# Optimization experiments

Hardware: AMD Instinct MI355X
Metric: run time of the kernel (lower is better)

## Reference

```python
import jax, jax.numpy as jnp
import numpy as np

B, S, D, H, K = 16, 4096, 256, 512, 3
EPS = 1e-5


def setup_inputs() -> dict:
    key = jax.random.key(0)
    ks = jax.random.split(key, 16)
    glorot = lambda k, shape: jax.random.uniform(
        k, shape, jnp.float32, -1.0, 1.0) * np.sqrt(6.0 / (shape[0] + shape[-1]))
    return {
        "inputs": jax.random.normal(ks[0], (B, S, D), jnp.float32),
        "mask": jax.random.randint(ks[1], (B, S), 0, 2, jnp.int32),
        "in_w": glorot(ks[2], (H, D)),
        "in_b": jnp.zeros((H,), jnp.float32),
        "gate_w": glorot(ks[3], (H, D)),
        "gate_b": jnp.zeros((H,), jnp.float32),
        "dw_w": glorot(ks[4], (H, 1, K)),
        "dw_b": jnp.zeros((H,), jnp.float32),
        "pw_w": glorot(ks[5], (H, H, 1)),
        "pw_b": jnp.zeros((H,), jnp.float32),
        "ln_g": jnp.ones((H,), jnp.float32),
        "ln_b": jnp.zeros((H,), jnp.float32),
        "A_log": jax.random.normal(ks[6], (H,), jnp.float32) * -0.1,
        "Bp": jax.random.normal(ks[7], (H,), jnp.float32) * 0.1,
        "Cp": jax.random.normal(ks[8], (H,), jnp.float32) * 0.1,
    }


def _forward(inputs, mask, in_w, in_b, gate_w, gate_b, dw_w, dw_b,
             pw_w, pw_b, ln_g, ln_b, A_log, Bp, Cp):
    # projections: torch Linear is x @ W.T + b
    x_lin = jnp.einsum('bsd,hd->bsh', inputs, in_w) + in_b
    g_lin = jnp.einsum('bsd,hd->bsh', inputs, gate_w) + gate_b
    h = jnp.tanh(x_lin)
    m_f = mask.astype(h.dtype)                      # [B,S]
    h = h * m_f[:, :, None]
    # depthwise conv over time: [B,H,S] with groups=H, 'same' padding
    pad = (K - 1) // 2
    h_t = jnp.transpose(h, (0, 2, 1))               # [B,H,S]
    h_conv = jax.lax.conv_general_dilated(
        h_t, dw_w, window_strides=(1,), padding=[(pad, pad)],
        dimension_numbers=('NCH', 'OIH', 'NCH'), feature_group_count=H)
    h_conv = h_conv + dw_b[None, :, None]
    h_conv = jnp.transpose(h_conv, (0, 2, 1))       # [B,S,H]
    # pointwise 1x1 conv
    h_conv = jnp.einsum('bsh,oh->bso', h_conv, pw_w[:, :, 0]) + pw_b
    u = jax.nn.silu(h_conv + h)
    g = jax.nn.sigmoid(g_lin)
    a_exp = jnp.exp(-jax.nn.softplus(A_log))        # [H]

    def step(carry, xs):
        state, last = carry
        ut, gt, mt = xs                             # [B,H],[B,H],[B]
        new_state = gt * (a_exp * state) + (1.0 - gt) * (Bp * ut)
        keep = (mt > 0.5)[:, None]
        state = jnp.where(keep, new_state, state)
        y = state * Cp
        last = jnp.where(keep, y, last)
        return (state, last), last

    init = (jnp.zeros((B, H), u.dtype), jnp.zeros((B, H), u.dtype))
    xs = (jnp.transpose(u, (1, 0, 2)), jnp.transpose(g, (1, 0, 2)),
          jnp.transpose(m_f, (1, 0)))
    _, y_seq = jax.lax.scan(step, init, xs)         # [S,B,H]
    y_seq = jnp.transpose(y_seq, (1, 0, 2))         # [B,S,H]
    # LayerNorm over last dim
    mu = jnp.mean(y_seq, axis=-1, keepdims=True)
    var = jnp.var(y_seq, axis=-1, keepdims=True)
    return (y_seq - mu) * jax.lax.rsqrt(var + EPS) * ln_g + ln_b


def reference(inputs, mask, in_w, in_b, gate_w, gate_b, dw_w, dw_b,
              pw_w, pw_b, ln_g, ln_b, A_log, Bp, Cp):
    return _forward(inputs, mask, in_w, in_b, gate_w, gate_b, dw_w, dw_b,
                    pw_w, pw_b, ln_g, ln_b, A_log, Bp, Cp)
```

## Files before the change

### kernel.cpp

```cpp
#include <hip/hip_runtime.h>
#include <hip/hip_bf16.h>
#include <math.h>

#define B_  16
#define S_  4096
#define D_  256
#define H_  512
#define BS_ 65536
#define BSH_ 33554432L
#define BSD_ 16777216L
#define CCH 128
#define LCH 32
#define TPAD 136

typedef __bf16 bf16;
typedef __bf16 bf16x8 __attribute__((ext_vector_type(8)));
typedef float  f32x4  __attribute__((ext_vector_type(4)));

#define AS1 __attribute__((address_space(1)))
#define AS3 __attribute__((address_space(3)))

__device__ __forceinline__ void gload_lds16(const void* g, void* l) {
  __builtin_amdgcn_global_load_lds((const AS1 void*)g, (AS3 void*)l, 16, 0, 0);
}

#if __has_builtin(__builtin_amdgcn_exp2f)
#define EXP2F __builtin_amdgcn_exp2f
#else
#define EXP2F exp2f
#endif
#if __has_builtin(__builtin_amdgcn_rcpf)
#define RCPF __builtin_amdgcn_rcpf
#else
#define RCPF(x) (1.f/(x))
#endif
#define L2E 1.4426950408889634f

__device__ __forceinline__ float fsigmoid(float x) {
  return RCPF(1.f + EXP2F(-L2E * x));
}
__device__ __forceinline__ float ftanh(float x) {
  return 2.f * RCPF(1.f + EXP2F(-2.f * L2E * x)) - 1.f;
}
__device__ __forceinline__ float fsilu(float x) {
  return x * RCPF(1.f + EXP2F(-L2E * x));
}

__global__ void k_cast_x(const float* __restrict__ x, bf16* __restrict__ xb, int n8) {
  int i = blockIdx.x * blockDim.x + threadIdx.x;
  if (i >= n8) return;
  const float4* p = (const float4*)x + (long)i * 2;
  float4 a = p[0], b = p[1];
  bf16x8 o;
  o[0]=(bf16)a.x; o[1]=(bf16)a.y; o[2]=(bf16)a.z; o[3]=(bf16)a.w;
  o[4]=(bf16)b.x; o[5]=(bf16)b.y; o[6]=(bf16)b.z; o[7]=(bf16)b.w;
  ((bf16x8*)xb)[i] = o;
}

__global__ void k_cast_w(const float* __restrict__ in_w, const float* __restrict__ gate_w,
                         const float* __restrict__ pw_w,
                         bf16* __restrict__ w1, bf16* __restrict__ pw) {
  int i = blockIdx.x * blockDim.x + threadIdx.x;
  const int HD = H_ * D_;
  if (i < HD)            w1[i] = (bf16)in_w[i];
  else if (i < 2 * HD)   w1[i] = (bf16)gate_w[i - HD];
  else {
    int j = i - 2 * HD;
    if (j < H_ * H_)     pw[j] = (bf16)pw_w[j];
  }
}

template<int KDIM, int EPI>
__global__ __launch_bounds__(512, 5)
void k_gemm(const bf16* __restrict__ A, const bf16* __restrict__ Bw,
            const int* __restrict__ mask,
            const float* __restrict__ bias0, const float* __restrict__ bias1,
            const bf16* __restrict__ hbuf, const bf16* __restrict__ gbuf,
            const float* __restrict__ A_log, const float* __restrict__ Bp,
            float* __restrict__ Ac, float* __restrict__ Bc,
            bf16* __restrict__ out0, bf16* __restrict__ out1, int Ntiles)
{
  extern __shared__ char smem_raw[];
  bf16* tile = (bf16*)smem_raw;

  const int t = threadIdx.x;
  const int w = t >> 6, lane = t & 63;
  const int nwg = gridDim.x;
  const int wg = (blockIdx.x & 7) * (nwg >> 3) + (blockIdx.x >> 3);
  const int bn0 = (wg % Ntiles) * 128;
  const int bm0 = (wg / Ntiles) * 128;
  const int wm = w >> 2, wn = w & 3;
  const int fr = lane & 15, kq = lane >> 4;
  constexpr int NT = KDIM / 32;

  const bf16* Ag = A  + (long)(bm0 + (t >> 2)) * KDIM + (t & 3) * 8;
  const bf16* Bg = Bw + (long)(bn0 + (t >> 2)) * KDIM + (t & 3) * 8;

  f32x4 acc[4][2];
#pragma unroll
  for (int i = 0; i < 4; ++i)
#pragma unroll
    for (int j = 0; j < 2; ++j) acc[i][j] = (f32x4){0.f, 0.f, 0.f, 0.f};

#define STAGE(tt)                                                           \
  { char* _b = smem_raw + ((tt) & 1) * 16384;                               \
    gload_lds16(Ag + (tt) * 32, (bf16*)_b + t * 8);                         \
    gload_lds16(Bg + (tt) * 32, (bf16*)(_b + 8192) + t * 8); }

  STAGE(0); STAGE(1);

#pragma unroll
  for (int kt = 0; kt < NT; ++kt) {
    if (kt + 1 < NT) asm volatile("s_waitcnt vmcnt(2)" ::: "memory");
    else             asm volatile("s_waitcnt vmcnt(0)" ::: "memory");
    __builtin_amdgcn_s_barrier();

    const bf16* As = (const bf16*)(smem_raw + (kt & 1) * 16384);
    const bf16* Bs = As + 4096;
    bf16x8 af[4], bfr[2];
#pragma unroll
    for (int mi = 0; mi < 4; ++mi)
      af[mi] = *(const bf16x8*)&As[(wm * 64 + mi * 16 + fr) * 32 + kq * 8];
#pragma unroll
    for (int ni = 0; ni < 2; ++ni)
      bfr[ni] = *(const bf16x8*)&Bs[(wn * 32 + ni * 16 + fr) * 32 + kq * 8];

    asm volatile("s_waitcnt lgkmcnt(0)" ::: "memory");
    __builtin_amdgcn_s_barrier();

    if (kt + 2 < NT) STAGE(kt + 2);

#pragma unroll
    for (int mi = 0; mi < 4; ++mi)
#pragma unroll
      for (int ni = 0; ni < 2; ++ni)
        acc[mi][ni] = __builtin_amdgcn_mfma_f32_16x16x32_bf16(af[mi], bfr[ni], acc[mi][ni], 0, 0, 0);
  }
#undef STAGE

  __syncthreads();

  const bool hside = (EPI != 1) || (bn0 < H_);
#pragma unroll
  for (int mi = 0; mi < 4; ++mi) {
#pragma unroll
    for (int rr = 0; rr < 4; ++rr) {
      const int row = wm * 64 + mi * 16 + kq * 4 + rr;
      const int gm = bm0 + row;
      float mf = 1.f;
      if (EPI == 1) mf = (mask[gm] != 0) ? 1.f : 0.f;
#pragma unroll
      for (int ni = 0; ni < 2; ++ni) {
        const int col = wn * 32 + ni * 16 + fr;
        float c = acc[mi][ni][rr];
        float val;
        if (EPI == 1) {
          const int gn = bn0 + col;
          val = hside ? ftanh(c + bias0[gn]) * mf
                      : fsigmoid(c + bias1[gn - H_]);
        } else {
          val = c + bias0[bn0 + col];
        }
        tile[row * TPAD + col] = (bf16)val;
      }
    }
  }
  __syncthreads();

  const int pr = t >> 4;
  const int pc = (t & 15) * 8;
#pragma unroll
  for (int rr = 0; rr < 4; ++rr) {
    const int row = pr + rr * 32;
    const long gm = bm0 + row;
    bf16x8 v = *(const bf16x8*)&tile[row * TPAD + pc];
    if (EPI == 1) {
      if (hside) *(bf16x8*)&out0[gm * H_ + bn0 + pc] = v;
      else       *(bf16x8*)&out1[gm * H_ + (bn0 - H_) + pc] = v;
    } else {
      bf16x8 hb = *(const bf16x8*)&hbuf[gm * H_ + bn0 + pc];
      bf16x8 o;
#pragma unroll
      for (int k = 0; k < 8; ++k) {
        float s = (float)v[k] + (float)hb[k];
        o[k] = (bf16)fsilu(s);
      }
      *(bf16x8*)&out0[gm * H_ + bn0 + pc] = o;
      *(bf16x8*)&tile[row * TPAD + pc] = o;
    }
  }

  if constexpr (EPI == 2) {
    __syncthreads();
    const int c_idx = t >> 7;
    const int col   = t & 127;
    const int gcol  = bn0 + col;
    const int bIdx  = bm0 >> 12;
    const int s0    = bm0 & (S_ - 1);
    const int chunk = (s0 >> 5) + c_idx;
    const int* mrow = mask + bIdx * S_ + s0 + c_idx * 32;
    const float aexp = RCPF(1.f + EXP2F(L2E * A_log[gcol]));
    const float bp = Bp[gcol];
    const bf16* grow = gbuf + (long)(bm0 + c_idx * 32) * H_ + gcol;
    float At = 1.f, Bt = 0.f;
#pragma unroll 4
    for (int sl = 0; sl < LCH; ++sl) {
      float uv = (float)tile[(c_idx * 32 + sl) * TPAD + col];
      float gv = (float)grow[(long)sl * H_];
      bool mm = mrow[sl] != 0;
      float a_s = mm ? gv * aexp : 1.f;
      float b_s = mm ? (1.f - gv) * (bp * uv) : 0.f;
      At = a_s * At;
      Bt = fmaf(a_s, Bt, b_s);
    }
    long o = ((long)chunk * B_ + bIdx) * H_ + gcol;
    Ac[o] = At; Bc[o] = Bt;
  }
}

__global__ void k_dwconv(const bf16* __restrict__ h, const float* __restrict__ dww,
                         const float* __restrict__ dwb, bf16* __restrict__ hc)
{
  long idx = (long)blockIdx.x * blockDim.x + threadIdx.x;
  long m = idx >> 6;
  int h8 = ((int)idx & 63) << 3;
  int s = (int)(m & (S_ - 1));
  bf16x8 c0, c1, c2;
#pragma unroll
  for (int j = 0; j < 8; ++j) { c0[j] = (bf16)0.f; c2[j] = (bf16)0.f; }
  if (s > 0)        c0 = *(const bf16x8*)(h + (m - 1) * H_ + h8);
  c1 = *(const bf16x8*)(h + m * H_ + h8);
  if (s < S_ - 1)   c2 = *(const bf16x8*)(h + (m + 1) * H_ + h8);
  bf16x8 o;
#pragma unroll
  for (int j = 0; j < 8; ++j) {
    int hh = h8 + j;
    float v = (float)c0[j] * dww[hh * 3 + 0] + (float)c1[j] * dww[hh * 3 + 1]
            + (float)c2[j] * dww[hh * 3 + 2] + dwb[hh];
    o[j] = (bf16)v;
  }
  *(bf16x8*)(hc + m * H_ + h8) = o;
}


__global__ __launch_bounds__(256)
void k_scan2(const float* __restrict__ Ac, const float* __restrict__ Bc,
             float* __restrict__ Sin)
{
  int tid = blockIdx.x * 256 + threadIdx.x;
  int b = tid >> 9, h = tid & (H_ - 1);
  const long stride = (long)B_ * H_;
  long o = (long)b * H_ + h;
  float st = 0.f;
  float a = Ac[o], bb = Bc[o];
  for (int c = 0; c < CCH; ++c) {
    float an = 0.f, bn = 0.f;
    if (c + 1 < CCH) { an = Ac[o + stride]; bn = Bc[o + stride]; }
    Sin[o] = st;
    st = fmaf(a, st, bb);
    a = an; bb = bn; o += stride;
  }
}

__global__ __launch_bounds__(512)
void k_scan3(const bf16* __restrict__ u, const bf16* __restrict__ g,
             const int* __restrict__ mask, const float* __restrict__ A_log,
             const float* __restrict__ Bp, const float* __restrict__ Cp,
             const float* __restrict__ Sin,
             const float* __restrict__ ln_g, const float* __restrict__ ln_b,
             float* __restrict__ out)
{
  __shared__ float ylds[LCH][H_];
  int c = blockIdx.x, b = blockIdx.y, h = threadIdx.x;
  float aexp = 1.f / (1.f + expf(A_log[h]));
  float bp = Bp[h], cp = Cp[h];
  float st = Sin[((long)c * B_ + b) * H_ + h];
  long base = ((long)b * S_ + (long)c * LCH) * H_ + h;
  const int* mrow = mask + b * S_ + c * LCH;
  for (int sl = 0; sl < LCH; ++sl) {
    float uv = (float)u[base + (long)sl * H_];
    float gv = (float)g[base + (long)sl * H_];
    bool mm = mrow[sl] != 0;
    float a_s = mm ? gv * aexp : 1.f;
    float b_s = mm ? (1.f - gv) * (bp * uv) : 0.f;
    st = fmaf(a_s, st, b_s);
    ylds[sl][h] = st * cp;
  }
  __syncthreads();
  int wv = h >> 6, ln = h & 63;
#pragma unroll
  for (int rr = 0; rr < 4; ++rr) {
    int row = wv * 4 + rr;
    float v[8];
    float sum = 0.f, sq = 0.f;
#pragma unroll
    for (int j = 0; j < 8; ++j) {
      v[j] = ylds[row][ln + 64 * j];
      sum += v[j]; sq += v[j] * v[j];
    }
#pragma unroll
    for (int off = 32; off; off >>= 1) {
      sum += __shfl_xor(sum, off);
      sq  += __shfl_xor(sq, off);
    }
    float mu = sum * (1.f / H_);
    float var = sq * (1.f / H_) - mu * mu;
    float rs = rsqrtf(var + 1e-5f);
    long ob = ((long)b * S_ + (long)c * LCH + row) * H_;
#pragma unroll
    for (int j = 0; j < 8; ++j) {
      int col = ln + 64 * j;
      out[ob + col] = (v[j] - mu) * rs * ln_g[col] + ln_b[col];
    }
  }
}

extern "C" void kernel_launch(void* const* d_in, const int* in_sizes, int n_in,
                              void* d_out, int out_size, void* d_ws, size_t ws_size,
                              hipStream_t stream)
{
  const float* x      = (const float*)d_in[0];
  const int*   mask   = (const int*)d_in[1];
  const float* in_w   = (const float*)d_in[2];
  const float* in_b   = (const float*)d_in[3];
  const float* gate_w = (const float*)d_in[4];
  const float* gate_b = (const float*)d_in[5];
  const float* dw_w   = (const float*)d_in[6];
  const float* dw_b   = (const float*)d_in[7];
  const float* pw_w   = (const float*)d_in[8];
  const float* pw_b   = (const float*)d_in[9];
  const float* ln_g   = (const float*)d_in[10];
  const float* ln_b   = (const float*)d_in[11];
  const float* A_log  = (const float*)d_in[12];
  const float* Bp     = (const float*)d_in[13];
  const float* Cp     = (const float*)d_in[14];

  char* ws = (char*)d_ws;
  bf16*  xb  = (bf16*)(ws + 0L);
  bf16*  h   = (bf16*)(ws + 33554432L);
  bf16*  hc  = (bf16*)(ws + 100663296L);
  bf16*  u   = (bf16*)(ws + 167772160L);
  bf16*  g   = (bf16*)(ws + 234881024L);
  bf16*  w1  = (bf16*)(ws + 301989888L);
  bf16*  pw  = (bf16*)(ws + 302514176L);
  float* Ac  = (float*)(ws + 303038464L);
  float* Bc  = (float*)(ws + 307232768L);
  float* Sin = (float*)(ws + 311427072L);
  float* out = (float*)d_out;

  const int gemm_lds = 128 * TPAD * 2;

  k_cast_x<<<8192, 256, 0, stream>>>(x, xb, (int)(BSD_ / 8));
  k_cast_w<<<2048, 256, 0, stream>>>(in_w, gate_w, pw_w, w1, pw);
  k_gemm<256, 1><<<512 * 8, 512, gemm_lds, stream>>>(
      xb, w1, mask, in_b, gate_b, nullptr, nullptr, nullptr, nullptr,
      nullptr, nullptr, h, g, 8);
  k_dwconv<<<16384, 256, 0, stream>>>(h, dw_w, dw_b, hc);
  k_gemm<512, 2><<<512 * 4, 512, gemm_lds, stream>>>(
      hc, pw, mask, pw_b, nullptr, h, g, A_log, Bp,
      Ac, Bc, u, nullptr, 4);
  k_scan2<<<32, 256, 0, stream>>>(Ac, Bc, Sin);
  k_scan3<<<dim3(CCH, B_), 512, 0, stream>>>(u, g, mask, A_log, Bp, Cp, Sin, ln_g, ln_b, out);
}
```

Measured before the change: 375.4 us.

## Restructure final scan so each wave owns a chunk and fuses LayerNorm per row

The final scan+LayerNorm kernel now gives each 64-lane wave one time chunk. Each lane handles 8 contiguous channels using bf16x8 vector loads, and the next row's u/g/mask values are software-prefetched. LayerNorm is computed per timestep with a wave-wide shuffle reduction and written with vectorized float4 stores. This removes the shared-memory staging buffer and the block barrier, and makes loads and stores wider. In exchange each thread holds more state in registers, and each block now carries four chunks instead of one. It depends on RCPF/EXP2F/L2E macros that are presumably defined in the unseen part of the file.

```diff
diff --git a/kernel.cpp b/kernel.cpp
--- a/kernel.cpp
+++ b/kernel.cpp
@@ -262,7 +262,7 @@
   }
 }
 
-__global__ __launch_bounds__(512)
+__global__ __launch_bounds__(256)
 void k_scan3(const bf16* __restrict__ u, const bf16* __restrict__ g,
              const int* __restrict__ mask, const float* __restrict__ A_log,
              const float* __restrict__ Bp, const float* __restrict__ Cp,
@@ -270,48 +270,63 @@
              const float* __restrict__ ln_g, const float* __restrict__ ln_b,
              float* __restrict__ out)
 {
-  __shared__ float ylds[LCH][H_];
-  int c = blockIdx.x, b = blockIdx.y, h = threadIdx.x;
-  float aexp = 1.f / (1.f + expf(A_log[h]));
-  float bp = Bp[h], cp = Cp[h];
-  float st = Sin[((long)c * B_ + b) * H_ + h];
-  long base = ((long)b * S_ + (long)c * LCH) * H_ + h;
+  const int wv = threadIdx.x >> 6, lane = threadIdx.x & 63;
+  const int c = blockIdx.x * 4 + wv;
+  const int b = blockIdx.y;
+  const int h0 = lane * 8;
+
+  float aexp[8], bp[8], cp[8], lg[8], lb[8], st[8];
+#pragma unroll
+  for (int j = 0; j < 8; ++j) {
+    aexp[j] = RCPF(1.f + EXP2F(L2E * A_log[h0 + j]));
+    bp[j] = Bp[h0 + j]; cp[j] = Cp[h0 + j];
+    lg[j] = ln_g[h0 + j]; lb[j] = ln_b[h0 + j];
+    st[j] = Sin[((long)c * B_ + b) * H_ + h0 + j];
+  }
+
+  const long base = ((long)b * S_ + (long)c * LCH) * H_ + h0;
   const int* mrow = mask + b * S_ + c * LCH;
+
+  bf16x8 uv = *(const bf16x8*)(u + base);
+  bf16x8 gv = *(const bf16x8*)(g + base);
+  int mm = mrow[0];
+
   for (int sl = 0; sl < LCH; ++sl) {
-    float uv = (float)u[base + (long)sl * H_];
-    float gv = (float)g[base + (long)sl * H_];
-    bool mm = mrow[sl] != 0;
-    float a_s = mm ? gv * aexp : 1.f;
-    float b_s = mm ? (1.f - gv) * (bp * uv) : 0.f;
-    st = fmaf(a_s, st, b_s);
-    ylds[sl][h] = st * cp;
-  }
-  __syncthreads();
-  int wv = h >> 6, ln = h & 63;
-#pragma unroll
-  for (int rr = 0; rr < 4; ++rr) {
-    int row = wv * 4 + rr;
-    float v[8];
-    float sum = 0.f, sq = 0.f;
+    bf16x8 un, gn; int mn = 0;
+    if (sl + 1 < LCH) {
+      un = *(const bf16x8*)(u + base + (long)(sl + 1) * H_);
+      gn = *(const bf16x8*)(g + base + (long)(sl + 1) * H_);
+      mn = mrow[sl + 1];
+    }
+    const bool m = mm != 0;
+    float y[8], sum = 0.f, sq = 0.f;
 #pragma unroll
     for (int j = 0; j < 8; ++j) {
-      v[j] = ylds[row][ln + 64 * j];
-      sum += v[j]; sq += v[j] * v[j];
+      float uu = (float)uv[j], gg = (float)gv[j];
+      float a_s = m ? gg * aexp[j] : 1.f;
+      float b_s = m ? (1.f - gg) * (bp[j] * uu) : 0.f;
+      st[j] = fmaf(a_s, st[j], b_s);
+      y[j] = st[j] * cp[j];
+      sum += y[j];
+      sq = fmaf(y[j], y[j], sq);
     }
 #pragma unroll
     for (int off = 32; off; off >>= 1) {
       sum += __shfl_xor(sum, off);
       sq  += __shfl_xor(sq, off);
     }
-    float mu = sum * (1.f / H_);
-    float var = sq * (1.f / H_) - mu * mu;
-    float rs = rsqrtf(var + 1e-5f);
-    long ob = ((long)b * S_ + (long)c * LCH + row) * H_;
-#pragma unroll
-    for (int j = 0; j < 8; ++j) {
-      int col = ln + 64 * j;
-      out[ob + col] = (v[j] - mu) * rs * ln_g[col] + ln_b[col];
-    }
+    const float mu = sum * (1.f / H_);
+    const float var = sq * (1.f / H_) - mu * mu;
+    const float rs = rsqrtf(var + 1e-5f);
+    const long ob = base + (long)sl * H_;
+    f32x4 o0, o1;
+#pragma unroll
+    for (int j = 0; j < 4; ++j) o0[j] = (y[j] - mu) * rs * lg[j] + lb[j];
+#pragma unroll
+    for (int j = 0; j < 4; ++j) o1[j] = (y[4 + j] - mu) * rs * lg[4 + j] + lb[4 + j];
+    *(f32x4*)(out + ob) = o0;
+    *(f32x4*)(out + ob + 4) = o1;
+    uv = un; gv = gn; mm = mn;
   }
 }
 
@@ -360,5 +375,6 @@
       hc, pw, mask, pw_b, nullptr, h, g, A_log, Bp,
       Ac, Bc, u, nullptr, 4);
   k_scan2<<<32, 256, 0, stream>>>(Ac, Bc, Sin);
-  k_scan3<<<dim3(CCH, B_), 512, 0, stream>>>(u, g, mask, A_log, Bp, Cp, Sin, ln_g, ln_b, out);
-}
+  k_scan3<<<dim3(CCH / 4, B_), 256, 0, stream>>>(
+      u, g, mask, A_log, Bp, Cp, Sin, ln_g, ln_b, out);
+}
```

Result: faster. 326.4 us (-13.0%).
